# Kernel optimization log

Hardware: AMD Instinct MI355X
Metric: run time of the kernel (lower is better)

## Reference

```python
import jax, jax.numpy as jnp
import numpy as np

EMBED_DIM = 384
B, P, N = 8, 4, 4096


def setup_inputs() -> dict:
    key = jax.random.key(0)
    k1, k2, k3, k4, k5 = jax.random.split(key, 5)
    scale = 1.0 / np.sqrt(EMBED_DIM)
    return {
        "x": jax.random.normal(k1, (B, EMBED_DIM, P, N), dtype=jnp.float32),
        "w_qkv": jax.random.normal(k2, (1 + 2 * EMBED_DIM, EMBED_DIM), dtype=jnp.float32) * scale,
        "b_qkv": jax.random.normal(k3, (1 + 2 * EMBED_DIM,), dtype=jnp.float32) * 0.01,
        "w_out": jax.random.normal(k4, (EMBED_DIM, EMBED_DIM), dtype=jnp.float32) * scale,
        "b_out": jax.random.normal(k5, (EMBED_DIM,), dtype=jnp.float32) * 0.01,
    }


def reference(x, w_qkv, b_qkv, w_out, b_out):
    # x: [B, C, P, N] (C=embed_dim, P=patch area, N=num patches)
    C = x.shape[1]
    # 1x1 conv qkv projection -> [B, 1+2C, P, N]
    qkv = jnp.einsum("bcpn,oc->bopn", x, w_qkv) + b_qkv[None, :, None, None]
    q = qkv[:, :1]            # [B, 1, P, N]
    k = qkv[:, 1:1 + C]       # [B, C, P, N]
    v = qkv[:, 1 + C:]        # [B, C, P, N]
    # softmax over spatial dim N (attn_dropout=0 -> identity)
    context_scores = jax.nn.softmax(q, axis=-1)
    # context vector: weighted sum over N -> [B, C, P, 1]
    context_vector = jnp.sum(k * context_scores, axis=-1, keepdims=True)
    # broadcast-multiply with relu(v)
    out = jax.nn.relu(v) * context_vector
    # 1x1 conv output projection
    out = jnp.einsum("bcpn,oc->bopn", out, w_out) + b_out[None, :, None, None]
    return out
```

## Files before the change

### kernel.cpp

```cpp
#include <hip/hip_runtime.h>
#include <hip/hip_bf16.h>
#include <stdint.h>

#define CC   384
#define BB   8
#define PP   4
#define NNN  4096
#define NBP  32
#define PN   (PP*NNN)

#define AS1 __attribute__((address_space(1)))
#define AS3 __attribute__((address_space(3)))

typedef float  f32x4 __attribute__((ext_vector_type(4)));
typedef short  s16x8 __attribute__((ext_vector_type(8)));
typedef unsigned short u16x4 __attribute__((ext_vector_type(4)));

__device__ __forceinline__ unsigned short f2bf(float f) {
  unsigned int u = __float_as_uint(f);
  u += 0x7fffu + ((u >> 16) & 1u);
  return (unsigned short)(u >> 16);
}
__device__ __forceinline__ float bf2f(unsigned short u) {
  return __uint_as_float(((unsigned int)u) << 16);
}

__device__ __forceinline__ int swz16(int r) {
  return ((r ^ (r >> 2)) & 15) << 4;
}

__device__ __forceinline__ void stage16(const char* g, char* l_uniform, int lane) {
#if defined(__has_builtin) && __has_builtin(__builtin_amdgcn_global_load_lds)
  __builtin_amdgcn_global_load_lds((const AS1 unsigned int*)g,
                                   (AS3 unsigned int*)l_uniform, 16, 0, 0);
#else
  *(int4*)(l_uniform + lane*16) = *(const int4*)g;
#endif
}


__global__ __launch_bounds__(256) void k_pre(
    const float* __restrict__ x, const float* __restrict__ wqkv,
    unsigned short* __restrict__ xbf, float* __restrict__ q)
{
  __shared__ __align__(16) unsigned short tr[24576];
  __shared__ float4 qw[64];
  char* trb = (char*)tr;
  const int bid = blockIdx.x;
  const int bp = bid >> 6, nt = bid & 63;
  const int b = bp >> 2, p = bp & 3;
  const int n0 = nt * 64;
  const int t  = threadIdx.x;
  const int wv_ = t >> 6, lane = t & 63;
  const int cg = t >> 4, nv = t & 15;
  const int r0 = 4 * nv;
  const float* xb = x + (size_t)b*CC*PN + (size_t)p*NNN + n0 + r0;
  const int s0 = swz16(r0+0), s1 = swz16(r0+1), s2 = swz16(r0+2), s3 = swz16(r0+3);

  float4 qa = {0.f, 0.f, 0.f, 0.f};
  #pragma unroll 3
  for (int it = 0; it < 12; ++it) {
    const int c0 = 32*it + 2*cg;
    const float4 x0 = *(const float4*)(xb + (size_t)c0*PN);
    const float4 x1 = *(const float4*)(xb + (size_t)(c0+1)*PN);
    const float w0 = wqkv[c0], w1 = wqkv[c0+1];
    qa.x += w0*x0.x + w1*x1.x;
    qa.y += w0*x0.y + w1*x1.y;
    qa.z += w0*x0.z + w1*x1.z;
    qa.w += w0*x0.w + w1*x1.w;
    const unsigned int p0 = (unsigned)f2bf(x0.x) | ((unsigned)f2bf(x1.x) << 16);
    const unsigned int p1 = (unsigned)f2bf(x0.y) | ((unsigned)f2bf(x1.y) << 16);
    const unsigned int p2 = (unsigned)f2bf(x0.z) | ((unsigned)f2bf(x1.z) << 16);
    const unsigned int p3 = (unsigned)f2bf(x0.w) | ((unsigned)f2bf(x1.w) << 16);
    const int cb = 2*c0;
    *(unsigned int*)(trb + (((r0+0)*768 + cb) ^ s0)) = p0;
    *(unsigned int*)(trb + (((r0+1)*768 + cb) ^ s1)) = p1;
    *(unsigned int*)(trb + (((r0+2)*768 + cb) ^ s2)) = p2;
    *(unsigned int*)(trb + (((r0+3)*768 + cb) ^ s3)) = p3;
  }
  qa.x += __shfl_xor(qa.x, 16); qa.y += __shfl_xor(qa.y, 16);
  qa.z += __shfl_xor(qa.z, 16); qa.w += __shfl_xor(qa.w, 16);
  qa.x += __shfl_xor(qa.x, 32); qa.y += __shfl_xor(qa.y, 32);
  qa.z += __shfl_xor(qa.z, 32); qa.w += __shfl_xor(qa.w, 32);
  if (lane < 16) qw[wv_*16 + lane] = qa;
  __syncthreads();
  const int4* trs = (const int4*)tr;
  int4* dst = (int4*)(xbf + (size_t)bid * 24576);
  #pragma unroll
  for (int j = 0; j < 12; ++j) dst[j*256 + t] = trs[j*256 + t];
  if (t < 16) {
    float4 a0 = qw[t], a1 = qw[16+t], a2 = qw[32+t], a3 = qw[48+t];
    float4 o; o.x = a0.x+a1.x+a2.x+a3.x; o.y = a0.y+a1.y+a2.y+a3.y;
    o.z = a0.z+a1.z+a2.z+a3.z; o.w = a0.w+a1.w+a2.w+a3.w;
    *(float4*)(q + (size_t)bp*NNN + n0 + 4*t) = o;
  }
}

__global__ __launch_bounds__(256) void k_wcvt2(
    const float* __restrict__ wqkv, const float* __restrict__ wout,
    unsigned short* __restrict__ wvt, unsigned short* __restrict__ woutt)
{
  const int i = blockIdx.x*256 + threadIdx.x;
  const int e = (i < CC*CC) ? i : i - CC*CC;
  const int j   = e & 7;
  const int g   = (e >> 3) & 3;
  const int l15 = (e >> 5) & 15;
  const int rem = e >> 9;
  const int ks  = rem % 12;
  const int mf  = rem / 12;
  const int row = 16*mf + l15;
  const int col = 32*ks + 8*g + j;
  if (i < CC*CC) wvt[e]          = f2bf(wqkv[(size_t)(385 + row)*CC + col]);
  else           woutt[e]        = f2bf(wout[(size_t)row*CC + col]);
}

__global__ __launch_bounds__(256) void k_softmax2(
    const float* __restrict__ q, const float* __restrict__ bqkv,
    float* __restrict__ scores)
{
  __shared__ float red[8];
  const int bp = blockIdx.x;
  const int t  = threadIdx.x;
  const int wv_ = t >> 6, ln = t & 63;
  const float bq = bqkv[0];
  float4 qv[4];
  float lmax = -1e30f;
  #pragma unroll
  for (int i = 0; i < 4; ++i) {
    const int n = i*1024 + t*4;
    float4 a = *(const float4*)(q + (size_t)bp*NNN + n);
    qv[i].x = a.x + bq; qv[i].y = a.y + bq; qv[i].z = a.z + bq; qv[i].w = a.w + bq;
    lmax = fmaxf(lmax, fmaxf(fmaxf(qv[i].x, qv[i].y), fmaxf(qv[i].z, qv[i].w)));
  }
  #pragma unroll
  for (int off = 32; off; off >>= 1) lmax = fmaxf(lmax, __shfl_xor(lmax, off));
  if (ln == 0) red[wv_] = lmax;
  __syncthreads();
  const float M = fmaxf(fmaxf(red[0], red[1]), fmaxf(red[2], red[3]));
  float lsum = 0.f;
  #pragma unroll
  for (int i = 0; i < 4; ++i) {
    qv[i].x = expf(qv[i].x - M); qv[i].y = expf(qv[i].y - M);
    qv[i].z = expf(qv[i].z - M); qv[i].w = expf(qv[i].w - M);
    lsum += qv[i].x + qv[i].y + qv[i].z + qv[i].w;
  }
  #pragma unroll
  for (int off = 32; off; off >>= 1) lsum += __shfl_xor(lsum, off);
  if (ln == 0) red[4 + wv_] = lsum;
  __syncthreads();
  const float inv = 1.f / (red[4] + red[5] + red[6] + red[7]);
  #pragma unroll
  for (int i = 0; i < 4; ++i) {
    const int n = i*1024 + t*4;
    float4 o; o.x=qv[i].x*inv; o.y=qv[i].y*inv; o.z=qv[i].z*inv; o.w=qv[i].w*inv;
    *(float4*)(scores + (size_t)bp*NNN + n) = o;
  }
}

__global__ __launch_bounds__(384) void k_xs2(
    const unsigned short* __restrict__ xbf, const float* __restrict__ scores,
    float* __restrict__ partial)
{
  __shared__ __align__(16) char lds[49152];
  __shared__ float sl[64];
  const int bid = blockIdx.x;
  const int bp = bid >> 6, nt = bid & 63;
  const int t = threadIdx.x;
  const int w6 = t >> 6, lane = t & 63;
  const char* gsrc = (const char*)xbf + (size_t)bid * 49152;
  #pragma unroll
  for (int r = 0; r < 8; ++r) {
    const int loff = (r*6 + w6) * 1024;
    stage16(gsrc + loff + lane*16, lds + loff, lane);
  }
  if (t < 64) sl[t] = scores[(size_t)bp*NNN + nt*64 + t];
  __syncthreads();
  float acc = 0.f;
  #pragma unroll 8
  for (int r = 0; r < 64; ++r) {
    const unsigned short uv = *(const unsigned short*)(lds + ((r*768 + 2*t) ^ swz16(r)));
    acc += bf2f(uv) * sl[r];
  }
  partial[(size_t)bid*CC + t] = acc;
}

__global__ __launch_bounds__(384) void k_cv2(
    const float* __restrict__ partial, const float* __restrict__ wqkv,
    const float* __restrict__ bqkv, float* __restrict__ cv)
{
  __shared__ float xsl[CC];
  const int bp = blockIdx.x;
  const int t  = threadIdx.x;
  float s = 0.f;
  #pragma unroll 8
  for (int nt = 0; nt < 64; ++nt) s += partial[((size_t)bp*64 + nt)*CC + t];
  xsl[t] = s;
  __syncthreads();
  float acc = bqkv[1 + t];
  const float* wk = wqkv + (size_t)(1 + t)*CC;
  #pragma unroll 8
  for (int c2 = 0; c2 < CC; ++c2) acc += wk[c2] * xsl[c2];
  cv[(size_t)bp*CC + t] = acc;
}

__device__ __forceinline__ void gemm_t2(
    const unsigned short* __restrict__ wt, const char* lds,
    int w, int g, int l15, f32x4 acc[2][8])
{
  const unsigned short* base = wt + (size_t)(2*w)*12*512 + l15*32 + g*8;
  s16x8 a[3][2];
  #pragma unroll
  for (int pf = 0; pf < 3; ++pf)
    #pragma unroll
    for (int mi = 0; mi < 2; ++mi)
      a[pf][mi] = *(const s16x8*)(base + ((size_t)mi*12 + pf)*512);
  #pragma unroll
  for (int ks = 0; ks < 12; ++ks) {
    const int slot = ks % 3;
    s16x8 bfr[8];
    #pragma unroll
    for (int nt = 0; nt < 8; ++nt) {
      const int row = 16*(nt & 3) + l15;
      const int byteb = (nt >> 2)*49152 + ((row*768 + 64*ks + 16*g) ^ swz16(row));
      bfr[nt] = *(const s16x8*)(lds + byteb);
    }
    #pragma unroll
    for (int mi = 0; mi < 2; ++mi)
      #pragma unroll
      for (int nt = 0; nt < 8; ++nt)
        acc[mi][nt] = __builtin_amdgcn_mfma_f32_16x16x32_bf16(
            a[slot][mi], bfr[nt], acc[mi][nt], 0, 0, 0);
    if (ks + 3 < 12) {
      #pragma unroll
      for (int mi = 0; mi < 2; ++mi)
        a[slot][mi] = *(const s16x8*)(base + ((size_t)mi*12 + ks + 3)*512);
    }
  }
}

__global__ __launch_bounds__(768, 1) void k_main2b(
    const unsigned short* __restrict__ xbf,
    const unsigned short* __restrict__ wvt,
    const unsigned short* __restrict__ woutt,
    const float* __restrict__ cv,
    const float* __restrict__ bqkv,
    const float* __restrict__ bout,
    float* __restrict__ out)
{
  __shared__ __align__(16) char lds[98304];
  const int bid = blockIdx.x;
  const int bp  = bid >> 5;
  const int t2  = bid & 31;
  const int b = bp >> 2, p = bp & 3;
  const int tid = threadIdx.x;
  const int w = tid >> 6;
  const int lane = tid & 63;
  const int g = lane >> 4, l15 = lane & 15;

  {
    const char* gsrc = (const char*)xbf + (size_t)(bp*64 + t2*2) * 49152;
    #pragma unroll
    for (int r = 0; r < 8; ++r) {
      const int loff = (r*12 + w) * 1024;
      stage16(gsrc + loff + lane*16, lds + loff, lane);
    }
  }
  __syncthreads();

  f32x4 acc[2][8];
  #pragma unroll
  for (int i = 0; i < 2; ++i)
    #pragma unroll
    for (int j = 0; j < 8; ++j) acc[i][j] = (f32x4){0.f,0.f,0.f,0.f};

  gemm_t2(wvt, lds, w, g, l15, acc);
  __syncthreads();

  const float* cvp = cv + (size_t)bp*CC;
  #pragma unroll
  for (int mi = 0; mi < 2; ++mi) {
    const int m0 = 32*w + 16*mi + 4*g;
    const float* bv = bqkv + 385 + m0;
    const float b0 = bv[0], b1 = bv[1], b2 = bv[2], b3 = bv[3];
    const float4 cvv = *(const float4*)(cvp + m0);
    #pragma unroll
    for (int nt = 0; nt < 8; ++nt) {
      const int row = 16*(nt & 3) + l15;
      const f32x4 t = acc[mi][nt];
      u16x4 pk = { f2bf(fmaxf(t[0]+b0, 0.f)*cvv.x), f2bf(fmaxf(t[1]+b1, 0.f)*cvv.y),
                   f2bf(fmaxf(t[2]+b2, 0.f)*cvv.z), f2bf(fmaxf(t[3]+b3, 0.f)*cvv.w) };
      const int byte0 = (nt >> 2)*49152 + ((row*768 + 2*m0) ^ swz16(row));
      *(u16x4*)(lds + byte0) = pk;
    }
  }
  __syncthreads();

  #pragma unroll
  for (int i = 0; i < 2; ++i)
    #pragma unroll
    for (int j = 0; j < 8; ++j) acc[i][j] = (f32x4){0.f,0.f,0.f,0.f};

  gemm_t2(woutt, lds, w, g, l15, acc);

  float* fl = (float*)lds;
  #pragma unroll
  for (int half = 0; half < 2; ++half) {
    __syncthreads();
    #pragma unroll
    for (int mi = 0; mi < 2; ++mi) {
      const int m0 = 32*w + 16*mi + 4*g;
      const float4 bo = *(const float4*)(bout + m0);
      const int cswz = g << 3;
      #pragma unroll
      for (int nt2 = 0; nt2 < 4; ++nt2) {
        const f32x4 t = acc[mi][4*half + nt2];
        const int colh = (16*nt2 + l15) ^ cswz;
        fl[(m0+0)*64 + colh] = t[0] + bo.x;
        fl[(m0+1)*64 + colh] = t[1] + bo.y;
        fl[(m0+2)*64 + colh] = t[2] + bo.z;
        fl[(m0+3)*64 + colh] = t[3] + bo.w;
      }
    }
    __syncthreads();
    float* outb = out + (size_t)b*CC*PN + (size_t)p*NNN + t2*128 + half*64;
    #pragma unroll
    for (int ps = 0; ps < 8; ++ps) {
      const int idx = ps*768 + tid;
      const int row = idx >> 4;
      const int nq  = idx & 15;
      const int qb  = (nq*4) ^ (((row >> 2) & 3) << 3);
      const f32x4 v = *(const f32x4*)(fl + row*64 + qb);
      __builtin_nontemporal_store(v, (f32x4*)(outb + (size_t)row*PN + nq*4));
    }
  }
}


__global__ __launch_bounds__(256) void k_qpart(
    const float* __restrict__ x, const float* __restrict__ wqkv,
    float* __restrict__ qpart)
{
  const int bid = blockIdx.x;
  const int seg = bid & 3;
  const int nc  = (bid >> 2) & 3;
  const int bp  = bid >> 4;
  const int b = bp >> 2, p = bp & 3;
  const int n = nc * 1024 + threadIdx.x * 4;
  const float* xb = x + (size_t)b*CC*PN + (size_t)p*NNN + n;
  float ax = 0.f, ay = 0.f, az = 0.f, aw = 0.f;
  const int c0 = seg * 96;
  #pragma unroll 8
  for (int c = c0; c < c0 + 96; ++c) {
    const float w = wqkv[c];
    const float4 xv = *(const float4*)(xb + (size_t)c*PN);
    ax += w*xv.x; ay += w*xv.y; az += w*xv.z; aw += w*xv.w;
  }
  float4 o; o.x=ax; o.y=ay; o.z=az; o.w=aw;
  *(float4*)(qpart + (size_t)(seg*NBP + bp)*NNN + n) = o;
}

__global__ __launch_bounds__(256) void k_softmax(
    const float* __restrict__ qpart, const float* __restrict__ bqkv,
    float* __restrict__ scores)
{
  __shared__ float red[8];
  const int bp = blockIdx.x;
  const int t  = threadIdx.x;
  const int wv_ = t >> 6, ln = t & 63;
  const float bq = bqkv[0];
  float4 q[4];
  float lmax = -1e30f;
  #pragma unroll
  for (int i = 0; i < 4; ++i) {
    const int n = i*1024 + t*4;
    const float* base = qpart + (size_t)bp*NNN + n;
    const float4 a = *(const float4*)(base);
    const float4 b1 = *(const float4*)(base + (size_t)NBP*NNN);
    const float4 c1 = *(const float4*)(base + (size_t)2*NBP*NNN);
    const float4 d1 = *(const float4*)(base + (size_t)3*NBP*NNN);
    q[i].x = a.x+b1.x+c1.x+d1.x + bq;
    q[i].y = a.y+b1.y+c1.y+d1.y + bq;
    q[i].z = a.z+b1.z+c1.z+d1.z + bq;
    q[i].w = a.w+b1.w+c1.w+d1.w + bq;
    lmax = fmaxf(lmax, fmaxf(fmaxf(q[i].x, q[i].y), fmaxf(q[i].z, q[i].w)));
  }
  #pragma unroll
  for (int off = 32; off; off >>= 1) lmax = fmaxf(lmax, __shfl_xor(lmax, off));
  if (ln == 0) red[wv_] = lmax;
  __syncthreads();
  const float M = fmaxf(fmaxf(red[0], red[1]), fmaxf(red[2], red[3]));
  float lsum = 0.f;
  #pragma unroll
  for (int i = 0; i < 4; ++i) {
    q[i].x = expf(q[i].x - M); q[i].y = expf(q[i].y - M);
    q[i].z = expf(q[i].z - M); q[i].w = expf(q[i].w - M);
    lsum += q[i].x + q[i].y + q[i].z + q[i].w;
  }
  #pragma unroll
  for (int off = 32; off; off >>= 1) lsum += __shfl_xor(lsum, off);
  if (ln == 0) red[4 + wv_] = lsum;
  __syncthreads();
  const float inv = 1.f / (red[4] + red[5] + red[6] + red[7]);
  #pragma unroll
  for (int i = 0; i < 4; ++i) {
    const int n = i*1024 + t*4;
    float4 o; o.x=q[i].x*inv; o.y=q[i].y*inv; o.z=q[i].z*inv; o.w=q[i].w*inv;
    *(float4*)(scores + (size_t)bp*NNN + n) = o;
  }
}

__global__ __launch_bounds__(256) void k_xs(
    const float* __restrict__ x, const float* __restrict__ scores,
    float* __restrict__ xs)
{
  __shared__ float red[4];
  const int c  = blockIdx.x;
  const int bp = blockIdx.y;
  const int b = bp >> 2, p = bp & 3;
  const float* xr = x + ((size_t)b*CC + c)*PN + (size_t)p*NNN;
  const float* sr = scores + (size_t)bp*NNN;
  float acc = 0.f;
  #pragma unroll
  for (int i = 0; i < 4; ++i) {
    const int n = i*1024 + threadIdx.x*4;
    const float4 xv = *(const float4*)(xr + n);
    const float4 sv = *(const float4*)(sr + n);
    acc += xv.x*sv.x + xv.y*sv.y + xv.z*sv.z + xv.w*sv.w;
  }
  #pragma unroll
  for (int off = 32; off; off >>= 1) acc += __shfl_xor(acc, off);
  if ((threadIdx.x & 63) == 0) red[threadIdx.x >> 6] = acc;
  __syncthreads();
  if (threadIdx.x == 0) xs[(size_t)bp*CC + c] = red[0]+red[1]+red[2]+red[3];
}

__global__ __launch_bounds__(256) void k_wcvt(
    const float* __restrict__ wqkv, const float* __restrict__ wout,
    unsigned short* __restrict__ wv, unsigned short* __restrict__ woutb)
{
  const int i = blockIdx.x*256 + threadIdx.x;
  if (i < CC*CC) wv[i] = f2bf(wqkv[385*CC + i]);
  else           woutb[i - CC*CC] = f2bf(wout[i - CC*CC]);
}

__global__ __launch_bounds__(384) void k_cv(
    const float* __restrict__ wqkv, const float* __restrict__ bqkv,
    const float* __restrict__ xs, float* __restrict__ cv)
{
  __shared__ float xsl[CC];
  const int bp = blockIdx.x;
  const int t  = threadIdx.x;
  xsl[t] = xs[(size_t)bp*CC + t];
  __syncthreads();
  float acc = bqkv[1 + t];
  const float* wk = wqkv + (size_t)(1 + t)*CC;
  #pragma unroll 8
  for (int c2 = 0; c2 < CC; ++c2) acc += wk[c2] * xsl[c2];
  cv[(size_t)bp*CC + t] = acc;
}

__device__ __forceinline__ void stage_load(
    const float* __restrict__ xb, int w, int chunk, float s[12])
{
  const int c0 = 96*chunk + 12*w;
  const float* xc = xb + (size_t)c0 * PN;
  #pragma unroll
  for (int k = 0; k < 12; ++k) s[k] = xc[(size_t)k * PN];
}

__device__ __forceinline__ void stage_write(
    char* lds, int w, int n, int chunk, const float s[12])
{
  const int swz = (n & 15) << 4;
  const int c0 = 96*chunk + 12*w;
  #pragma unroll
  for (int j = 0; j < 3; ++j) {
    u16x4 pk = { f2bf(s[4*j]), f2bf(s[4*j+1]), f2bf(s[4*j+2]), f2bf(s[4*j+3]) };
    const int byte0 = (n*768 + 2*(c0 + 4*j)) ^ swz;
    *(u16x4*)(lds + byte0) = pk;
  }
}

template<int KSN>
__device__ __forceinline__ void gemm_ks(
    const unsigned short* __restrict__ wa, const char* lds,
    int w, int g, int l15, int ks0, f32x4 acc[3][4])
{
  const unsigned short* wb = wa + (size_t)(48*w + l15)*CC + 8*g;
  s16x8 afr[2][3];
  #pragma unroll
  for (int mi = 0; mi < 3; ++mi)
    afr[0][mi] = *(const s16x8*)(wb + (size_t)(16*mi)*CC + 32*ks0);
  #pragma unroll
  for (int i = 0; i < KSN; ++i) {
    const int ks  = ks0 + i;
    const int cur = i & 1;
    if (i + 1 < KSN) {
      #pragma unroll
      for (int mi = 0; mi < 3; ++mi)
        afr[cur ^ 1][mi] = *(const s16x8*)(wb + (size_t)(16*mi)*CC + 32*(ks+1));
    }
    s16x8 bfr[4];
    #pragma unroll
    for (int nt = 0; nt < 4; ++nt) {
      const int row = 16*nt + l15;
      const int byteb = (row*768 + 64*ks + 16*g) ^ (l15 << 4);
      bfr[nt] = *(const s16x8*)(lds + byteb);
    }
    #pragma unroll
    for (int mi = 0; mi < 3; ++mi)
      #pragma unroll
      for (int nt = 0; nt < 4; ++nt)
        acc[mi][nt] = __builtin_amdgcn_mfma_f32_16x16x32_bf16(
            afr[cur][mi], bfr[nt], acc[mi][nt], 0, 0, 0);
  }
}

__global__ __launch_bounds__(512, 4) void k_main(
    const float* __restrict__ x,
    const unsigned short* __restrict__ wv,
    const unsigned short* __restrict__ woutb,
    const float* __restrict__ cv,
    const float* __restrict__ bqkv,
    const float* __restrict__ bout,
    float* __restrict__ out)
{
  __shared__ __align__(16) unsigned short lds_u16[64*384];
  char* lds = (char*)lds_u16;
  const int bid = blockIdx.x;
  const int nb  = bid & 63;
  const int bp  = bid >> 6;
  const int b = bp >> 2, p = bp & 3;
  const int n0 = nb * 64;
  const int tid  = threadIdx.x;
  const int w    = tid >> 6;
  const int lane = tid & 63;
  const int g    = lane >> 4;
  const int l15  = lane & 15;

  const float* xb = x + (size_t)b*CC*PN + (size_t)p*NNN + n0 + lane;

  float s[12];
  stage_load(xb, w, 0, s);
  stage_write(lds, w, lane, 0, s);
  stage_load(xb, w, 1, s);
  __syncthreads();

  f32x4 acc[3][4];
  #pragma unroll
  for (int i = 0; i < 3; ++i)
    #pragma unroll
    for (int j = 0; j < 4; ++j) acc[i][j] = (f32x4){0.f,0.f,0.f,0.f};

  for (int c = 0; c < 4; ++c) {
    gemm_ks<3>(wv, lds, w, g, l15, 3*c, acc);
    if (c < 3) {
      stage_write(lds, w, lane, c+1, s);
      if (c < 2) stage_load(xb, w, c+2, s);
    }
    __syncthreads();
  }

  const float* cvp = cv + (size_t)bp*CC;
  #pragma unroll
  for (int mi = 0; mi < 3; ++mi) {
    const int m0 = 48*w + 16*mi + 4*g;
    const float* bv = bqkv + 385 + m0;
    const float b0 = bv[0], b1 = bv[1], b2 = bv[2], b3 = bv[3];
    const float4 cvv = *(const float4*)(cvp + m0);
    #pragma unroll
    for (int nt = 0; nt < 4; ++nt) {
      const int row = 16*nt + l15;
      const f32x4 t = acc[mi][nt];
      u16x4 pk = { f2bf(fmaxf(t[0]+b0, 0.f)*cvv.x), f2bf(fmaxf(t[1]+b1, 0.f)*cvv.y),
                   f2bf(fmaxf(t[2]+b2, 0.f)*cvv.z), f2bf(fmaxf(t[3]+b3, 0.f)*cvv.w) };
      const int byte0 = (row*768 + 2*m0) ^ (l15 << 4);
      *(u16x4*)(lds + byte0) = pk;
    }
  }
  __syncthreads();

  #pragma unroll
  for (int i = 0; i < 3; ++i)
    #pragma unroll
    for (int j = 0; j < 4; ++j) acc[i][j] = (f32x4){0.f,0.f,0.f,0.f};

  gemm_ks<12>(woutb, lds, w, g, l15, 0, acc);

  #pragma unroll
  for (int mi = 0; mi < 3; ++mi) {
    const int m0 = 48*w + 16*mi + 4*g;
    const float4 bo = *(const float4*)(bout + m0);
    #pragma unroll
    for (int nt = 0; nt < 4; ++nt) {
      const int nn = n0 + 16*nt + l15;
      const f32x4 t = acc[mi][nt];
      float* ob = out + ((size_t)b*CC + m0)*PN + (size_t)p*NNN + nn;
      ob[0]            = t[0] + bo.x;
      ob[(size_t)PN]   = t[1] + bo.y;
      ob[2*(size_t)PN] = t[2] + bo.z;
      ob[3*(size_t)PN] = t[3] + bo.w;
    }
  }
}

extern "C" void kernel_launch(void* const* d_in, const int* in_sizes, int n_in,
                              void* d_out, int out_size, void* d_ws, size_t ws_size,
                              hipStream_t stream) {
  const float* x    = (const float*)d_in[0];
  const float* wqkv = (const float*)d_in[1];
  const float* bqkv = (const float*)d_in[2];
  const float* wout = (const float*)d_in[3];
  const float* bout = (const float*)d_in[4];
  float* out = (float*)d_out;
  char* ws = (char*)d_ws;

  const size_t OFF_XBF = 0;
  const size_t OFF_Q   = 100663296;
  const size_t OFF_SC  = 101187584;
  const size_t OFF_PT  = 101711872;
  const size_t OFF_WVT = 104857600;
  const size_t OFF_WOT = 105152512;
  const size_t OFF_CV  = 105447424;
  const size_t NEED    = 105496576;

  if (ws_size >= NEED) {
    unsigned short* xbf   = (unsigned short*)(ws + OFF_XBF);
    float* q              = (float*)(ws + OFF_Q);
    float* scores         = (float*)(ws + OFF_SC);
    float* partial        = (float*)(ws + OFF_PT);
    unsigned short* wvt   = (unsigned short*)(ws + OFF_WVT);
    unsigned short* woutt = (unsigned short*)(ws + OFF_WOT);
    float* cvp            = (float*)(ws + OFF_CV);

    hipLaunchKernelGGL(k_pre,      dim3(2048), dim3(256), 0, stream, x, wqkv, xbf, q);
    hipLaunchKernelGGL(k_wcvt2,    dim3(1152), dim3(256), 0, stream, wqkv, wout, wvt, woutt);
    hipLaunchKernelGGL(k_softmax2, dim3(32),   dim3(256), 0, stream, q, bqkv, scores);
    hipLaunchKernelGGL(k_xs2,      dim3(2048), dim3(384), 0, stream, xbf, scores, partial);
    hipLaunchKernelGGL(k_cv2,      dim3(32),   dim3(384), 0, stream, partial, wqkv, bqkv, cvp);
    hipLaunchKernelGGL(k_main2b,   dim3(1024), dim3(768), 0, stream, xbf, wvt, woutt, cvp, bqkv, bout, out);
  } else {
    float* scores         = (float*)(ws);
    float* qpart          = (float*)(ws + 524288);
    float* xs             = (float*)(ws + 2621440);
    unsigned short* wv    = (unsigned short*)(ws + 2719744);
    unsigned short* woutb = (unsigned short*)(ws + 3014656);
    float* cvp            = (float*)(ws + 3309568);

    hipLaunchKernelGGL(k_qpart,   dim3(512),      dim3(256), 0, stream, x, wqkv, qpart);
    hipLaunchKernelGGL(k_wcvt,    dim3(1152),     dim3(256), 0, stream, wqkv, wout, wv, woutb);
    hipLaunchKernelGGL(k_softmax, dim3(32),       dim3(256), 0, stream, qpart, bqkv, scores);
    hipLaunchKernelGGL(k_xs,      dim3(CC, NBP),  dim3(256), 0, stream, x, scores, xs);
    hipLaunchKernelGGL(k_cv,      dim3(NBP),      dim3(384), 0, stream, wqkv, bqkv, xs, cvp);
    hipLaunchKernelGGL(k_main,    dim3(2048),     dim3(512), 0, stream, x, wv, woutb, cvp, bqkv, bout, out);
  }
}
```

Measured before the change: 233.3 us.

## Fuse tile-local softmax-weighted x reduction into k_pre with online rescaling

Computes per-tile max and exp-weighted partial sums of x directly from the LDS transpose buffer inside k_pre. This eliminates the k_xs2 kernel, which re-read the whole bf16 copy of x. The global softmax max and normaliser are then applied in k_cv3 by rescaling each tile's partial with exp(tile_max + bias - M). The cost is extra compute and synchronisation in k_pre, and bf16 precision is kept on the x values.

```diff
diff --git a/kernel.cpp b/kernel.cpp
--- a/kernel.cpp
+++ b/kernel.cpp
@@ -41,10 +41,14 @@
 
 __global__ __launch_bounds__(256) void k_pre(
     const float* __restrict__ x, const float* __restrict__ wqkv,
-    unsigned short* __restrict__ xbf, float* __restrict__ q)
+    unsigned short* __restrict__ xbf, float* __restrict__ q,
+    float* __restrict__ partial, float* __restrict__ mt)
 {
   __shared__ __align__(16) unsigned short tr[24576];
   __shared__ float4 qw[64];
+  __shared__ float4 qfin4[16];
+  __shared__ float e_sh[64];
+  __shared__ float m_sh;
   char* trb = (char*)tr;
   const int bid = blockIdx.x;
   const int bp = bid >> 6, nt = bid & 63;
@@ -93,6 +97,26 @@
     float4 o; o.x = a0.x+a1.x+a2.x+a3.x; o.y = a0.y+a1.y+a2.y+a3.y;
     o.z = a0.z+a1.z+a2.z+a3.z; o.w = a0.w+a1.w+a2.w+a3.w;
     *(float4*)(q + (size_t)bp*NNN + n0 + 4*t) = o;
+    qfin4[t] = o;
+    float m4 = fmaxf(fmaxf(o.x, o.y), fmaxf(o.z, o.w));
+    #pragma unroll
+    for (int off = 8; off; off >>= 1) m4 = fmaxf(m4, __shfl_xor(m4, off));
+    if (t == 0) { m_sh = m4; mt[bid] = m4; }
+  }
+  __syncthreads();
+  if (t < 64) {
+    const float* qf = (const float*)qfin4;
+    e_sh[t] = expf(qf[t] - m_sh);
+  }
+  __syncthreads();
+  for (int c = t; c < CC; c += 256) {
+    float acc = 0.f;
+    #pragma unroll 8
+    for (int r = 0; r < 64; ++r) {
+      const unsigned short uv = *(const unsigned short*)(trb + ((r*768 + 2*c) ^ swz16(r)));
+      acc += bf2f(uv) * e_sh[r];
+    }
+    partial[(size_t)bid*CC + c] = acc;
   }
 }
 
@@ -114,9 +138,9 @@
   else           woutt[e]        = f2bf(wout[(size_t)row*CC + col]);
 }
 
-__global__ __launch_bounds__(256) void k_softmax2(
+__global__ __launch_bounds__(256) void k_qmz(
     const float* __restrict__ q, const float* __restrict__ bqkv,
-    float* __restrict__ scores)
+    float* __restrict__ MZ)
 {
   __shared__ float red[8];
   const int bp = blockIdx.x;
@@ -140,61 +164,38 @@
   float lsum = 0.f;
   #pragma unroll
   for (int i = 0; i < 4; ++i) {
-    qv[i].x = expf(qv[i].x - M); qv[i].y = expf(qv[i].y - M);
-    qv[i].z = expf(qv[i].z - M); qv[i].w = expf(qv[i].w - M);
-    lsum += qv[i].x + qv[i].y + qv[i].z + qv[i].w;
+    lsum += expf(qv[i].x - M) + expf(qv[i].y - M)
+          + expf(qv[i].z - M) + expf(qv[i].w - M);
   }
   #pragma unroll
   for (int off = 32; off; off >>= 1) lsum += __shfl_xor(lsum, off);
   if (ln == 0) red[4 + wv_] = lsum;
   __syncthreads();
-  const float inv = 1.f / (red[4] + red[5] + red[6] + red[7]);
-  #pragma unroll
-  for (int i = 0; i < 4; ++i) {
-    const int n = i*1024 + t*4;
-    float4 o; o.x=qv[i].x*inv; o.y=qv[i].y*inv; o.z=qv[i].z*inv; o.w=qv[i].w*inv;
-    *(float4*)(scores + (size_t)bp*NNN + n) = o;
-  }
-}
-
-__global__ __launch_bounds__(384) void k_xs2(
-    const unsigned short* __restrict__ xbf, const float* __restrict__ scores,
-    float* __restrict__ partial)
-{
-  __shared__ __align__(16) char lds[49152];
-  __shared__ float sl[64];
-  const int bid = blockIdx.x;
-  const int bp = bid >> 6, nt = bid & 63;
-  const int t = threadIdx.x;
-  const int w6 = t >> 6, lane = t & 63;
-  const char* gsrc = (const char*)xbf + (size_t)bid * 49152;
-  #pragma unroll
-  for (int r = 0; r < 8; ++r) {
-    const int loff = (r*6 + w6) * 1024;
-    stage16(gsrc + loff + lane*16, lds + loff, lane);
-  }
-  if (t < 64) sl[t] = scores[(size_t)bp*NNN + nt*64 + t];
-  __syncthreads();
-  float acc = 0.f;
-  #pragma unroll 8
-  for (int r = 0; r < 64; ++r) {
-    const unsigned short uv = *(const unsigned short*)(lds + ((r*768 + 2*t) ^ swz16(r)));
-    acc += bf2f(uv) * sl[r];
-  }
-  partial[(size_t)bid*CC + t] = acc;
-}
-
-__global__ __launch_bounds__(384) void k_cv2(
-    const float* __restrict__ partial, const float* __restrict__ wqkv,
-    const float* __restrict__ bqkv, float* __restrict__ cv)
+  if (t == 0) {
+    MZ[2*bp]   = M;
+    MZ[2*bp+1] = red[4] + red[5] + red[6] + red[7];
+  }
+}
+
+__global__ __launch_bounds__(384) void k_cv3(
+    const float* __restrict__ partial, const float* __restrict__ mt,
+    const float* __restrict__ MZ, const float* __restrict__ bqkv,
+    const float* __restrict__ wqkv, float* __restrict__ cv)
 {
   __shared__ float xsl[CC];
+  __shared__ float esc[64];
   const int bp = blockIdx.x;
   const int t  = threadIdx.x;
+  const float bq = bqkv[0];
+  const float M = MZ[2*bp];
+  const float invZ = 1.f / MZ[2*bp+1];
+  if (t < 64) esc[t] = expf(mt[bp*64 + t] + bq - M);
+  __syncthreads();
   float s = 0.f;
   #pragma unroll 8
-  for (int nt = 0; nt < 64; ++nt) s += partial[((size_t)bp*64 + nt)*CC + t];
-  xsl[t] = s;
+  for (int t2 = 0; t2 < 64; ++t2)
+    s += partial[((size_t)bp*64 + t2)*CC + t] * esc[t2];
+  xsl[t] = s * invZ;
   __syncthreads();
   float acc = bqkv[1 + t];
   const float* wk = wqkv + (size_t)(1 + t)*CC;
@@ -617,28 +618,29 @@
 
   const size_t OFF_XBF = 0;
   const size_t OFF_Q   = 100663296;
-  const size_t OFF_SC  = 101187584;
-  const size_t OFF_PT  = 101711872;
-  const size_t OFF_WVT = 104857600;
-  const size_t OFF_WOT = 105152512;
-  const size_t OFF_CV  = 105447424;
-  const size_t NEED    = 105496576;
+  const size_t OFF_PT  = 101187584;
+  const size_t OFF_WVT = 104333312;
+  const size_t OFF_WOT = 104628224;
+  const size_t OFF_CV  = 104923136;
+  const size_t OFF_MT  = 104972288;
+  const size_t OFF_MZ  = 104980480;
+  const size_t NEED    = 104980736;
 
   if (ws_size >= NEED) {
     unsigned short* xbf   = (unsigned short*)(ws + OFF_XBF);
     float* q              = (float*)(ws + OFF_Q);
-    float* scores         = (float*)(ws + OFF_SC);
     float* partial        = (float*)(ws + OFF_PT);
     unsigned short* wvt   = (unsigned short*)(ws + OFF_WVT);
     unsigned short* woutt = (unsigned short*)(ws + OFF_WOT);
     float* cvp            = (float*)(ws + OFF_CV);
-
-    hipLaunchKernelGGL(k_pre,      dim3(2048), dim3(256), 0, stream, x, wqkv, xbf, q);
-    hipLaunchKernelGGL(k_wcvt2,    dim3(1152), dim3(256), 0, stream, wqkv, wout, wvt, woutt);
-    hipLaunchKernelGGL(k_softmax2, dim3(32),   dim3(256), 0, stream, q, bqkv, scores);
-    hipLaunchKernelGGL(k_xs2,      dim3(2048), dim3(384), 0, stream, xbf, scores, partial);
-    hipLaunchKernelGGL(k_cv2,      dim3(32),   dim3(384), 0, stream, partial, wqkv, bqkv, cvp);
-    hipLaunchKernelGGL(k_main2b,   dim3(1024), dim3(768), 0, stream, xbf, wvt, woutt, cvp, bqkv, bout, out);
+    float* mt             = (float*)(ws + OFF_MT);
+    float* MZ             = (float*)(ws + OFF_MZ);
+
+    hipLaunchKernelGGL(k_pre,    dim3(2048), dim3(256), 0, stream, x, wqkv, xbf, q, partial, mt);
+    hipLaunchKernelGGL(k_wcvt2,  dim3(1152), dim3(256), 0, stream, wqkv, wout, wvt, woutt);
+    hipLaunchKernelGGL(k_qmz,    dim3(32),   dim3(256), 0, stream, q, bqkv, MZ);
+    hipLaunchKernelGGL(k_cv3,    dim3(32),   dim3(384), 0, stream, partial, mt, MZ, bqkv, wqkv, cvp);
+    hipLaunchKernelGGL(k_main2b, dim3(1024), dim3(768), 0, stream, xbf, wvt, woutt, cvp, bqkv, bout, out);
   } else {
     float* scores         = (float*)(ws);
     float* qpart          = (float*)(ws + 524288);
```

After: 225.1 us. -3.5%, faster.
